# Kernel optimization log

Measured on AMD Instinct MI355X. Metric: run time of the kernel, lower is better.

## Reference

```python
import jax, jax.numpy as jnp
import numpy as np

N, L, E, H = 4, 2048, 512, 8
D = E // H


def setup_inputs() -> dict:
    key = jax.random.key(0)
    ks = jax.random.split(key, 8)
    causal = jnp.tril(jnp.ones((L, L), dtype=bool))[None, None]  # [1,1,L,L]
    return {
        "values": jax.random.normal(ks[0], (N, L, E), dtype=jnp.float32),
        "keys": jax.random.normal(ks[1], (N, L, E), dtype=jnp.float32),
        "query": jax.random.normal(ks[2], (N, L, E), dtype=jnp.float32),
        "mask": causal,
        "Wv": jax.random.normal(ks[3], (D, D), dtype=jnp.float32) * 0.05,
        "Wk": jax.random.normal(ks[4], (D, D), dtype=jnp.float32) * 0.05,
        "Wq": jax.random.normal(ks[5], (D, D), dtype=jnp.float32) * 0.05,
        "Wo": jax.random.normal(ks[6], (E, E), dtype=jnp.float32) * 0.05,
        "bo": jnp.zeros((E,), dtype=jnp.float32),
    }


def reference(values, keys, query, mask, Wv, Wk, Wq, Wo, bo):
    n, ql, e = query.shape
    # split heads: [N, len, H, D]
    v = values.reshape(n, -1, H, D)
    k = keys.reshape(n, -1, H, D)
    q = query.reshape(n, ql, H, D)
    # per-head linear projections (nn.Linear: x @ W.T, no bias)
    v = jnp.einsum("nlhd,od->nlho", v, Wv)
    k = jnp.einsum("nlhd,od->nlho", k, Wk)
    q = jnp.einsum("nqhd,od->nqho", q, Wq)
    # scores [N, H, Q, K]
    energy = jnp.einsum("nqhd,nkhd->nhqk", q, k)
    energy = jnp.where(mask == 0, jnp.float32(-1e28), energy)
    # NOTE: module scales by embed_size**0.5, not head_dim**0.5 (faithful)
    attn = jax.nn.softmax(energy / np.float32(e ** 0.5), axis=3)
    out = jnp.einsum("nhqk,nkhd->nqhd", attn, v).reshape(n, ql, e)
    return out @ Wo.T + bo
```

## Files before the change

kernel.cpp:

```cpp
#include <hip/hip_runtime.h>

#define NB 4
#define LL 2048
#define EE 512
#define HH 8
#define DD 64

typedef __attribute__((ext_vector_type(8))) short short8;
typedef __attribute__((ext_vector_type(4))) float f32x4;
typedef __attribute__((ext_vector_type(16))) float f32x16;
typedef __attribute__((ext_vector_type(4))) unsigned int u32x4;
typedef __attribute__((ext_vector_type(2))) int i32x2;
typedef __bf16 bf16x8 __attribute__((ext_vector_type(8)));

#if __has_builtin(__builtin_amdgcn_exp2f)
#define EXP2(x) __builtin_amdgcn_exp2f(x)
#else
#define EXP2(x) __expf((x) * 0.6931471805599453f)
#endif

#define QSCALE (0.04419417382415922f * 1.4426950408889634f)

static __device__ __forceinline__ short bfc(float f) {
    return __builtin_bit_cast(short, (__bf16)f);
}

static __device__ __forceinline__ unsigned pkbf(float lo, float hi) {
    unsigned short a = (unsigned short)(unsigned)__builtin_bit_cast(unsigned short, (__bf16)lo);
    unsigned short b = (unsigned short)(unsigned)__builtin_bit_cast(unsigned short, (__bf16)hi);
    return (unsigned)a | ((unsigned)b << 16);
}

#if __has_builtin(__builtin_amdgcn_permlane32_swap)
static __device__ __forceinline__ float plmax(float v) {
    i32x2 r = __builtin_amdgcn_permlane32_swap(
        __builtin_bit_cast(int, v), __builtin_bit_cast(int, v), false, false);
    return fmaxf(__builtin_bit_cast(float, r[0]), __builtin_bit_cast(float, r[1]));
}
#else
static __device__ __forceinline__ float plmax(float v) { return fmaxf(v, __shfl_xor(v, 32)); }
#endif

static __device__ __forceinline__ f32x4 mfma16(short8 a, short8 b, f32x4 c) {
    return __builtin_amdgcn_mfma_f32_16x16x32_bf16(
        __builtin_bit_cast(bf16x8, a), __builtin_bit_cast(bf16x8, b), c, 0, 0, 0);
}

static __device__ __forceinline__ f32x16 mfma32(short8 a, short8 b, f32x16 c) {
    return __builtin_amdgcn_mfma_f32_32x32x16_bf16(
        __builtin_bit_cast(bf16x8, a), __builtin_bit_cast(bf16x8, b), c, 0, 0, 0);
}

__global__ __launch_bounds__(256) void k_cvt(const float* __restrict__ src,
                                             unsigned short* __restrict__ dst, int n) {
    int i = (blockIdx.x * 256 + threadIdx.x) * 4;
    if (i < n) {
        float4 v = *(const float4*)(src + i);
        dst[i + 0] = (unsigned short)bfc(v.x);
        dst[i + 1] = (unsigned short)bfc(v.y);
        dst[i + 2] = (unsigned short)bfc(v.z);
        dst[i + 3] = (unsigned short)bfc(v.w);
    }
}

__global__ __launch_bounds__(256) void k_proj(const float* __restrict__ vals,
                                              const float* __restrict__ keys,
                                              const float* __restrict__ qry,
                                              const float* __restrict__ Wv,
                                              const float* __restrict__ Wk,
                                              const float* __restrict__ Wq,
                                              unsigned short* __restrict__ Qp,
                                              unsigned short* __restrict__ Kp,
                                              unsigned short* __restrict__ Vg) {
    __shared__ __align__(16) unsigned short kq[2][8256];
    __shared__ __align__(16) unsigned short vv[10272];

    const int tid = threadIdx.x;
    const int w = tid >> 6, ln = tid & 63;
    const int c = ln & 15, g = ln >> 4;
    const int r0 = blockIdx.x * 128;
    const int n = r0 >> 14;
    const int l0 = (r0 >> 3) & (LL - 1);
    const int h = c & 7;

    short8 xf[3][2][2];
    const float* Xs[3] = {vals, keys, qry};
#pragma unroll
    for (int t = 0; t < 3; ++t)
#pragma unroll
        for (int rt = 0; rt < 2; ++rt) {
            const int r = r0 + w * 32 + rt * 16 + c;
#pragma unroll
            for (int kk = 0; kk < 2; ++kk) {
                const float* p = Xs[t] + (size_t)r * DD + kk * 32 + g * 8;
                short8 v;
#pragma unroll
                for (int j = 0; j < 8; ++j) v[j] = bfc(p[j]);
                xf[t][rt][kk] = v;
            }
        }

#pragma unroll
    for (int t = 0; t < 3; ++t) {
        const float* W = (t == 0) ? Wv : (t == 1) ? Wk : Wq;
        short8 wf[4][2];
#pragma unroll
        for (int nt = 0; nt < 4; ++nt)
#pragma unroll
            for (int kk = 0; kk < 2; ++kk) {
                const float* p = W + (nt * 16 + c) * DD + kk * 32 + g * 8;
                short8 v;
#pragma unroll
                for (int j = 0; j < 8; ++j) v[j] = bfc(p[j]);
                wf[nt][kk] = v;
            }
#pragma unroll
        for (int rt = 0; rt < 2; ++rt) {
            const int l15 = w * 4 + rt * 2 + (c >> 3);
#pragma unroll
            for (int nt = 0; nt < 4; ++nt) {
                f32x4 acc = {0.f, 0.f, 0.f, 0.f};
                acc = mfma16(wf[nt][0], xf[t][rt][0], acc);
                acc = mfma16(wf[nt][1], xf[t][rt][1], acc);
                const int o = nt * 16 + g * 4;
                if (t == 0) {
#pragma unroll
                    for (int reg = 0; reg < 4; ++reg)
                        vv[h * 1284 + (o + reg) * 20 + l15] = (unsigned short)bfc(acc[reg]);
                } else {
                    const float s = (t == 2) ? QSCALE : 1.0f;
                    uint2 u = {pkbf(acc[0] * s, acc[1] * s), pkbf(acc[2] * s, acc[3] * s)};
                    *(uint2*)&kq[t - 1][h * 1032 + l15 * 64 + o] = u;
                }
            }
        }
    }
    __syncthreads();

#pragma unroll
    for (int t = 0; t < 2; ++t) {
        unsigned short* dstb = t ? Qp : Kp;
        const int hh = tid >> 5, s = tid & 31;
#pragma unroll
        for (int i = 0; i < 4; ++i) {
            const int q = s * 4 + i;
            const int l = q >> 3, cc = q & 7;
            uint4 v = *(const uint4*)&kq[t][hh * 1032 + l * 64 + cc * 8];
            *(uint4*)(dstb + ((size_t)(n * HH + hh) * LL + l0 + l) * DD + cc * 8) = v;
        }
    }

#pragma unroll
    for (int pi = 0; pi < 2; ++pi) {
        const int p = tid + pi * 256;
        const int hh = p >> 6, d = p & 63;
        const unsigned short* sp = &vv[hh * 1284 + d * 20];
        uint2 r0v = *(const uint2*)(sp + 0);
        uint2 r1v = *(const uint2*)(sp + 4);
        uint2 r2v = *(const uint2*)(sp + 8);
        uint2 r3v = *(const uint2*)(sp + 12);
        u32x4 o0 = {r0v.x, r0v.y, r1v.x, r1v.y};
        u32x4 o1 = {r2v.x, r2v.y, r3v.x, r3v.y};
        unsigned short* dst = Vg + (size_t)(n * HH + hh) * (LL * DD) +
                              (size_t)(l0 >> 4) * 1024 + d * 16;
        *(u32x4*)dst = o0;
        *(u32x4*)(dst + 8) = o1;
    }
}

static __device__ __forceinline__ void stage_tile(const unsigned short* __restrict__ src,
                                                  unsigned short* buf, int w, int ln,
                                                  size_t rstride) {
#pragma unroll
    for (int r = 0; r < 2; ++r) {
        int qi = w * 2 + r;
        int row = qi * 8 + (ln >> 3);
        int s = (ln & 7) ^ (row & 7);
        __builtin_amdgcn_global_load_lds(
            (const __attribute__((address_space(1))) unsigned int*)(src + (size_t)row * rstride + s * 8),
            (__attribute__((address_space(3))) unsigned int*)(buf + qi * 512),
            16, 0, 0);
    }
}

static __device__ __forceinline__ void stage_v(const unsigned short* __restrict__ src,
                                               unsigned short* buf, int w, int ln) {
#pragma unroll
    for (int r = 0; r < 2; ++r) {
        int idx = w * 64 + ln + r * 256;
        int d = idx >> 3, c16 = idx & 7;
        int cc = c16 ^ (d & 7);
        __builtin_amdgcn_global_load_lds(
            (const __attribute__((address_space(1))) unsigned int*)(src + (cc >> 1) * 1024 + d * 16 + (cc & 1) * 8),
            (__attribute__((address_space(3))) unsigned int*)(buf + idx * 8),
            16, 0, 0);
    }
}

__global__ __launch_bounds__(256, 4) void k_attn(const unsigned short* __restrict__ Qp,
                                                 const unsigned short* __restrict__ Kp,
                                                 const unsigned short* __restrict__ Vg,
                                                 unsigned short* __restrict__ Xa) {
    __shared__ __align__(16) unsigned short Kt[2][64 * 64];
    __shared__ __align__(16) unsigned short Vt[2][64 * 64];

    const int tid = threadIdx.x;
    const int w = tid >> 6, ln = tid & 63;
    const int c31 = ln & 31, g2 = ln >> 5;
    const int qpair = w >> 1, kvh = w & 1;

    const int b = blockIdx.x;
    const int x8 = b & 7;
    const int idx = b >> 3;
    const int nh = (x8 << 2) | (idx & 3);
    const int jj = (idx >> 2) & 15;
    const int j = (idx >> 6) ? jj : 31 - jj;
    const int qt = 2 * j + qpair;
    const int Q0 = qt * 32;
    const int nIter = j + 1;

    const unsigned short* Qb = Qp + (size_t)nh * (LL * DD);
    const unsigned short* Kb = Kp + (size_t)nh * (LL * DD);
    const unsigned short* Vb = Vg + (size_t)nh * (LL * DD);

    short8 qf[4];
#pragma unroll
    for (int kc = 0; kc < 4; ++kc)
        qf[kc] = *(const short8*)(Qb + (Q0 + c31) * DD + kc * 16 + g2 * 8);

    f32x16 oacc0, oacc1;
#pragma unroll
    for (int r = 0; r < 16; ++r) { oacc0[r] = 0.f; oacc1[r] = 0.f; }
    float m = -1e30f, lsum = 0.f;

    stage_tile(Kb, &Kt[0][0], w, ln, DD);
    stage_v(Vb, &Vt[0][0], w, ln);
    __syncthreads();

    int cur = 0;
    for (int t = 0; t < nIter; ++t) {
        const int nxt = cur ^ 1;
        if (t + 1 < nIter) {
            stage_tile(Kb + (size_t)(t + 1) * (64 * DD), &Kt[nxt][0], w, ln, DD);
            stage_v(Vb + (size_t)(t + 1) * 4096, &Vt[nxt][0], w, ln);
        }

        const int kb32 = t * 64 + kvh * 32;
        if (kb32 <= Q0 + 31) {
            const char* kb_ = (const char*)&Kt[cur][0];
            const char* vb_ = (const char*)&Vt[cur][0];
            const int q = Q0 + c31;

            f32x16 sc;
#pragma unroll
            for (int r = 0; r < 16; ++r) sc[r] = 0.f;
            {
                const int R = kvh * 32 + c31;
                const unsigned rb = (unsigned)(R * 128);
                const unsigned swz = (unsigned)((R & 7) << 4);
                __builtin_amdgcn_s_setprio(1);
#pragma unroll
                for (int kc = 0; kc < 4; ++kc) {
                    short8 af = *(const short8*)(kb_ + rb + (((unsigned)(kc * 32 + g2 * 16)) ^ swz));
                    sc = mfma32(af, qf[kc], sc);
                }
                __builtin_amdgcn_s_setprio(0);
            }

            if (kb32 + 31 > Q0) {
#pragma unroll
                for (int r = 0; r < 16; ++r) {
                    int kvg = kb32 + (r & 3) + 8 * (r >> 2) + 4 * g2;
                    sc[r] = (kvg > q) ? -1e30f : sc[r];
                }
            }

            float tm;
            {
                float a[8];
#pragma unroll
                for (int r = 0; r < 8; ++r) a[r] = fmaxf(sc[r], sc[r + 8]);
                float b0 = fmaxf(a[0], a[4]), b1 = fmaxf(a[1], a[5]);
                float b2 = fmaxf(a[2], a[6]), b3 = fmaxf(a[3], a[7]);
                tm = fmaxf(fmaxf(b0, b1), fmaxf(b2, b3));
            }
            tm = plmax(tm);

            if (!__all(tm <= m + 6.0f)) {
                float mn = fmaxf(m, tm);
                float corr = EXP2(m - mn);
                m = mn;
                lsum *= corr;
#pragma unroll
                for (int r = 0; r < 16; ++r) { oacc0[r] *= corr; oacc1[r] *= corr; }
            }

#pragma unroll
            for (int r = 0; r < 16; ++r) sc[r] = EXP2(sc[r] - m);
            {
                float a[8];
#pragma unroll
                for (int r = 0; r < 8; ++r) a[r] = sc[r] + sc[r + 8];
                float b0 = a[0] + a[4], b1 = a[1] + a[5];
                float b2 = a[2] + a[6], b3 = a[3] + a[7];
                lsum += (b0 + b1) + (b2 + b3);
            }

            unsigned pk[8];
#pragma unroll
            for (int iw = 0; iw < 8; ++iw) pk[iw] = pkbf(sc[2 * iw], sc[2 * iw + 1]);
#pragma unroll
            for (int ck = 0; ck < 2; ++ck) {
                unsigned s0 = g2 ? pk[4 * ck + 0] : pk[4 * ck + 2];
                unsigned s1 = g2 ? pk[4 * ck + 1] : pk[4 * ck + 3];
                unsigned x0 = __shfl_xor(s0, 32);
                unsigned x1 = __shfl_xor(s1, 32);
                u32x4 bfv;
                bfv[0] = g2 ? x0 : pk[4 * ck + 0];
                bfv[1] = g2 ? x1 : pk[4 * ck + 1];
                bfv[2] = g2 ? pk[4 * ck + 2] : x0;
                bfv[3] = g2 ? pk[4 * ck + 3] : x1;
                short8 pB = __builtin_bit_cast(short8, bfv);
                const unsigned coff = (unsigned)(kvh * 64 + ck * 32 + g2 * 16);
                __builtin_amdgcn_s_setprio(1);
                {
                    const int dP = c31;
                    short8 A = *(const short8*)(vb_ + (unsigned)(dP * 128) +
                                                (coff ^ ((unsigned)((dP & 7) << 4))));
                    oacc0 = mfma32(A, pB, oacc0);
                }
                {
                    const int dP = 32 + c31;
                    short8 A = *(const short8*)(vb_ + (unsigned)(dP * 128) +
                                                (coff ^ ((unsigned)((dP & 7) << 4))));
                    oacc1 = mfma32(A, pB, oacc1);
                }
                __builtin_amdgcn_s_setprio(0);
            }
        }

        __syncthreads();
        cur = nxt;
    }

    {
        float* mb = (float*)(&Kt[0][0]);
        float* lb = mb + 128;
        float* ob = (float*)(&Vt[0][0]);
        if (g2 == 0) mb[(qpair * 2 + kvh) * 32 + c31] = m;
        __syncthreads();
        const float mo = mb[(qpair * 2 + (kvh ^ 1)) * 32 + c31];
        const float alpha = EXP2(m - fmaxf(m, mo));
        lsum *= alpha;
#pragma unroll
        for (int r = 0; r < 16; ++r) { oacc0[r] *= alpha; oacc1[r] *= alpha; }
        if (kvh) {
            float* op = ob + qpair * 2048;
#pragma unroll
            for (int r = 0; r < 16; ++r) {
                op[r * 64 + ln] = oacc0[r];
                op[(16 + r) * 64 + ln] = oacc1[r];
            }
            lb[qpair * 64 + ln] = lsum;
        }
        __syncthreads();
        if (kvh) return;
        {
            const float* op = ob + qpair * 2048;
#pragma unroll
            for (int r = 0; r < 16; ++r) {
                oacc0[r] += op[r * 64 + ln];
                oacc1[r] += op[(16 + r) * 64 + ln];
            }
            lsum += lb[qpair * 64 + ln];
        }
    }

    lsum += __shfl_xor(lsum, 32);
    const float inv = 1.0f / lsum;
    const int n = nh >> 3, h = nh & 7;
    unsigned short* orow = Xa + ((size_t)(n * LL + Q0 + c31)) * EE + h * DD;
#pragma unroll
    for (int a = 0; a < 4; ++a) {
        {
            float e0 = oacc0[4 * a + 0] * inv, e1 = oacc0[4 * a + 1] * inv;
            float e2 = oacc0[4 * a + 2] * inv, e3 = oacc0[4 * a + 3] * inv;
            uint2 u = {pkbf(e0, e1), pkbf(e2, e3)};
            *(uint2*)(orow + a * 8 + g2 * 4) = u;
        }
        {
            float e0 = oacc1[4 * a + 0] * inv, e1 = oacc1[4 * a + 1] * inv;
            float e2 = oacc1[4 * a + 2] * inv, e3 = oacc1[4 * a + 3] * inv;
            uint2 u = {pkbf(e0, e1), pkbf(e2, e3)};
            *(uint2*)(orow + 32 + a * 8 + g2 * 4) = u;
        }
    }
}

__global__ __launch_bounds__(256) void k_out(const unsigned short* __restrict__ X,
                                             const unsigned short* __restrict__ Wob,
                                             const float* __restrict__ bo,
                                             float* __restrict__ out) {
    const int tid = threadIdx.x, w = tid >> 6, ln = tid & 63, c = ln & 15, g = ln >> 4;
    const int b = blockIdx.x;
    const int x8 = b & 7, jj = b >> 3;
    const int mb = x8 * 8 + (jj & 7);
    const int nb = jj >> 3;
    const int mbase = mb * 128 + w * 16;
    const int nbase = nb * 64;

    f32x4 acc0[4] = {}, acc1[4] = {};
    for (int ks = 0; ks < 16; ++ks) {
        short8 a0 = *(const short8*)(X + (size_t)(mbase + c) * EE + ks * 32 + g * 8);
        short8 a1 = *(const short8*)(X + (size_t)(mbase + 64 + c) * EE + ks * 32 + g * 8);
#pragma unroll
        for (int nt = 0; nt < 4; ++nt) {
            short8 bfr = *(const short8*)(Wob + (size_t)(nbase + nt * 16 + c) * EE + ks * 32 + g * 8);
            acc0[nt] = mfma16(a0, bfr, acc0[nt]);
            acc1[nt] = mfma16(a1, bfr, acc1[nt]);
        }
    }
#pragma unroll
    for (int nt = 0; nt < 4; ++nt) {
        float bias = bo[nbase + nt * 16 + c];
#pragma unroll
        for (int reg = 0; reg < 4; ++reg) {
            int row0 = mbase + g * 4 + reg;
            out[(size_t)row0 * EE + nbase + nt * 16 + c] = acc0[nt][reg] + bias;
            out[(size_t)(row0 + 64) * EE + nbase + nt * 16 + c] = acc1[nt][reg] + bias;
        }
    }
}

extern "C" void kernel_launch(void* const* d_in, const int* in_sizes, int n_in,
                              void* d_out, int out_size, void* d_ws, size_t ws_size,
                              hipStream_t stream) {
    const float* vals = (const float*)d_in[0];
    const float* keys = (const float*)d_in[1];
    const float* qry  = (const float*)d_in[2];
    const float* Wv = (const float*)d_in[4];
    const float* Wk = (const float*)d_in[5];
    const float* Wq = (const float*)d_in[6];
    const float* Wo = (const float*)d_in[7];
    const float* bo = (const float*)d_in[8];
    float* out = (float*)d_out;

    char* ws = (char*)d_ws;
    unsigned short* Qp  = (unsigned short*)(ws);
    unsigned short* Kp  = (unsigned short*)(ws + (8u  << 20));
    unsigned short* Vg  = (unsigned short*)(ws + (16u << 20));
    unsigned short* Xa  = (unsigned short*)(ws + (24u << 20));
    unsigned short* Wob = (unsigned short*)(ws + (32u << 20));

    hipLaunchKernelGGL(k_cvt, dim3(256), dim3(256), 0, stream, Wo, Wob, EE * EE);
    hipLaunchKernelGGL(k_proj, dim3(512), dim3(256), 0, stream,
                       vals, keys, qry, Wv, Wk, Wq, Qp, Kp, Vg);
    hipLaunchKernelGGL(k_attn, dim3(1024), dim3(256), 0, stream, Qp, Kp, Vg, Xa);
    hipLaunchKernelGGL(k_out, dim3(512), dim3(256), 0, stream, Xa, Wob, bo, out);
}
```

Before: 98.74 us.

## Fold Wo conversion into projection kernel, split K/Q and V blocks, prefetch in k_out

Removes the separate Wo fp32-to-bf16 conversion launch by folding it into the projection kernel's first 512 blocks. The projection grid doubles: half the blocks project K and Q, the other half project V, sharing one smaller LDS buffer, with launch bounds raised to allow four blocks per CU. The output GEMM gains register double-buffering, so the next k-step's A/B fragments load while the current MFMAs run. This trims launch overhead and improves occupancy and latency hiding, at the cost of more registers in k_out and duplicated per-block work such as reloading the W fragments.

```diff
diff --git a/kernel.cpp b/kernel.cpp
--- a/kernel.cpp
+++ b/kernel.cpp
@@ -51,120 +51,159 @@
         __builtin_bit_cast(bf16x8, a), __builtin_bit_cast(bf16x8, b), c, 0, 0, 0);
 }
 
-__global__ __launch_bounds__(256) void k_cvt(const float* __restrict__ src,
-                                             unsigned short* __restrict__ dst, int n) {
-    int i = (blockIdx.x * 256 + threadIdx.x) * 4;
-    if (i < n) {
-        float4 v = *(const float4*)(src + i);
-        dst[i + 0] = (unsigned short)bfc(v.x);
-        dst[i + 1] = (unsigned short)bfc(v.y);
-        dst[i + 2] = (unsigned short)bfc(v.z);
-        dst[i + 3] = (unsigned short)bfc(v.w);
-    }
-}
-
-__global__ __launch_bounds__(256) void k_proj(const float* __restrict__ vals,
-                                              const float* __restrict__ keys,
-                                              const float* __restrict__ qry,
-                                              const float* __restrict__ Wv,
-                                              const float* __restrict__ Wk,
-                                              const float* __restrict__ Wq,
-                                              unsigned short* __restrict__ Qp,
-                                              unsigned short* __restrict__ Kp,
-                                              unsigned short* __restrict__ Vg) {
-    __shared__ __align__(16) unsigned short kq[2][8256];
-    __shared__ __align__(16) unsigned short vv[10272];
+__global__ __launch_bounds__(256, 4) void k_proj(const float* __restrict__ vals,
+                                                 const float* __restrict__ keys,
+                                                 const float* __restrict__ qry,
+                                                 const float* __restrict__ Wv,
+                                                 const float* __restrict__ Wk,
+                                                 const float* __restrict__ Wq,
+                                                 const float* __restrict__ Wo,
+                                                 unsigned short* __restrict__ Qp,
+                                                 unsigned short* __restrict__ Kp,
+                                                 unsigned short* __restrict__ Vg,
+                                                 unsigned short* __restrict__ Wob) {
+    __shared__ __align__(16) unsigned short smem[16512];
 
     const int tid = threadIdx.x;
     const int w = tid >> 6, ln = tid & 63;
     const int c = ln & 15, g = ln >> 4;
-    const int r0 = blockIdx.x * 128;
-    const int n = r0 >> 14;
-    const int l0 = (r0 >> 3) & (LL - 1);
-    const int h = c & 7;
-
-    short8 xf[3][2][2];
-    const float* Xs[3] = {vals, keys, qry};
-#pragma unroll
-    for (int t = 0; t < 3; ++t)
+
+    if (blockIdx.x < 512) {
+        {
+            const int i = blockIdx.x * 512 + tid * 2;
+            float2 v = *(const float2*)(Wo + i);
+            Wob[i] = (unsigned short)bfc(v.x);
+            Wob[i + 1] = (unsigned short)bfc(v.y);
+        }
+        unsigned short (*kq)[8256] = (unsigned short (*)[8256])smem;
+        const int r0 = blockIdx.x * 128;
+        const int n = r0 >> 14;
+        const int l0 = (r0 >> 3) & (LL - 1);
+        const int h = c & 7;
+
+#pragma unroll
+        for (int t = 0; t < 2; ++t) {
+            const float* X = t ? qry : keys;
+            const float* W = t ? Wq : Wk;
+
+            short8 xf[2][2];
+#pragma unroll
+            for (int rt = 0; rt < 2; ++rt) {
+                const int r = r0 + w * 32 + rt * 16 + c;
+#pragma unroll
+                for (int kk = 0; kk < 2; ++kk) {
+                    const float* p = X + (size_t)r * DD + kk * 32 + g * 8;
+                    short8 v;
+#pragma unroll
+                    for (int j = 0; j < 8; ++j) v[j] = bfc(p[j]);
+                    xf[rt][kk] = v;
+                }
+            }
+            short8 wf[4][2];
+#pragma unroll
+            for (int nt = 0; nt < 4; ++nt)
+#pragma unroll
+                for (int kk = 0; kk < 2; ++kk) {
+                    const float* p = W + (nt * 16 + c) * DD + kk * 32 + g * 8;
+                    short8 v;
+#pragma unroll
+                    for (int j = 0; j < 8; ++j) v[j] = bfc(p[j]);
+                    wf[nt][kk] = v;
+                }
+
+#pragma unroll
+            for (int rt = 0; rt < 2; ++rt) {
+                const int l15 = w * 4 + rt * 2 + (c >> 3);
+#pragma unroll
+                for (int nt = 0; nt < 4; ++nt) {
+                    f32x4 acc = {0.f, 0.f, 0.f, 0.f};
+                    acc = mfma16(wf[nt][0], xf[rt][0], acc);
+                    acc = mfma16(wf[nt][1], xf[rt][1], acc);
+                    const int o = nt * 16 + g * 4;
+                    const float s = t ? QSCALE : 1.0f;
+                    uint2 u = {pkbf(acc[0] * s, acc[1] * s), pkbf(acc[2] * s, acc[3] * s)};
+                    *(uint2*)&kq[t][h * 1032 + l15 * 64 + o] = u;
+                }
+            }
+        }
+        __syncthreads();
+
+#pragma unroll
+        for (int t = 0; t < 2; ++t) {
+            unsigned short* dstb = t ? Qp : Kp;
+            const int hh = tid >> 5, s = tid & 31;
+#pragma unroll
+            for (int i = 0; i < 4; ++i) {
+                const int q = s * 4 + i;
+                const int l = q >> 3, cc = q & 7;
+                uint4 v = *(const uint4*)&kq[t][hh * 1032 + l * 64 + cc * 8];
+                *(uint4*)(dstb + ((size_t)(n * HH + hh) * LL + l0 + l) * DD + cc * 8) = v;
+            }
+        }
+    } else {
+        unsigned short* vv = smem;
+        const int r0 = (blockIdx.x - 512) * 128;
+        const int n = r0 >> 14;
+        const int l0 = (r0 >> 3) & (LL - 1);
+        const int h = c & 15 & 7;
+
+        short8 xf[2][2];
 #pragma unroll
         for (int rt = 0; rt < 2; ++rt) {
             const int r = r0 + w * 32 + rt * 16 + c;
 #pragma unroll
             for (int kk = 0; kk < 2; ++kk) {
-                const float* p = Xs[t] + (size_t)r * DD + kk * 32 + g * 8;
+                const float* p = vals + (size_t)r * DD + kk * 32 + g * 8;
                 short8 v;
 #pragma unroll
                 for (int j = 0; j < 8; ++j) v[j] = bfc(p[j]);
-                xf[t][rt][kk] = v;
-            }
-        }
-
-#pragma unroll
-    for (int t = 0; t < 3; ++t) {
-        const float* W = (t == 0) ? Wv : (t == 1) ? Wk : Wq;
+                xf[rt][kk] = v;
+            }
+        }
         short8 wf[4][2];
 #pragma unroll
         for (int nt = 0; nt < 4; ++nt)
 #pragma unroll
             for (int kk = 0; kk < 2; ++kk) {
-                const float* p = W + (nt * 16 + c) * DD + kk * 32 + g * 8;
+                const float* p = Wv + (nt * 16 + c) * DD + kk * 32 + g * 8;
                 short8 v;
 #pragma unroll
                 for (int j = 0; j < 8; ++j) v[j] = bfc(p[j]);
                 wf[nt][kk] = v;
             }
+
 #pragma unroll
         for (int rt = 0; rt < 2; ++rt) {
             const int l15 = w * 4 + rt * 2 + (c >> 3);
 #pragma unroll
             for (int nt = 0; nt < 4; ++nt) {
                 f32x4 acc = {0.f, 0.f, 0.f, 0.f};
-                acc = mfma16(wf[nt][0], xf[t][rt][0], acc);
-                acc = mfma16(wf[nt][1], xf[t][rt][1], acc);
+                acc = mfma16(wf[nt][0], xf[rt][0], acc);
+                acc = mfma16(wf[nt][1], xf[rt][1], acc);
                 const int o = nt * 16 + g * 4;
-                if (t == 0) {
-#pragma unroll
-                    for (int reg = 0; reg < 4; ++reg)
-                        vv[h * 1284 + (o + reg) * 20 + l15] = (unsigned short)bfc(acc[reg]);
-                } else {
-                    const float s = (t == 2) ? QSCALE : 1.0f;
-                    uint2 u = {pkbf(acc[0] * s, acc[1] * s), pkbf(acc[2] * s, acc[3] * s)};
-                    *(uint2*)&kq[t - 1][h * 1032 + l15 * 64 + o] = u;
-                }
-            }
-        }
-    }
-    __syncthreads();
-
-#pragma unroll
-    for (int t = 0; t < 2; ++t) {
-        unsigned short* dstb = t ? Qp : Kp;
-        const int hh = tid >> 5, s = tid & 31;
-#pragma unroll
-        for (int i = 0; i < 4; ++i) {
-            const int q = s * 4 + i;
-            const int l = q >> 3, cc = q & 7;
-            uint4 v = *(const uint4*)&kq[t][hh * 1032 + l * 64 + cc * 8];
-            *(uint4*)(dstb + ((size_t)(n * HH + hh) * LL + l0 + l) * DD + cc * 8) = v;
-        }
-    }
-
-#pragma unroll
-    for (int pi = 0; pi < 2; ++pi) {
-        const int p = tid + pi * 256;
-        const int hh = p >> 6, d = p & 63;
-        const unsigned short* sp = &vv[hh * 1284 + d * 20];
-        uint2 r0v = *(const uint2*)(sp + 0);
-        uint2 r1v = *(const uint2*)(sp + 4);
-        uint2 r2v = *(const uint2*)(sp + 8);
-        uint2 r3v = *(const uint2*)(sp + 12);
-        u32x4 o0 = {r0v.x, r0v.y, r1v.x, r1v.y};
-        u32x4 o1 = {r2v.x, r2v.y, r3v.x, r3v.y};
-        unsigned short* dst = Vg + (size_t)(n * HH + hh) * (LL * DD) +
-                              (size_t)(l0 >> 4) * 1024 + d * 16;
-        *(u32x4*)dst = o0;
-        *(u32x4*)(dst + 8) = o1;
+#pragma unroll
+                for (int reg = 0; reg < 4; ++reg)
+                    vv[h * 1284 + (o + reg) * 20 + l15] = (unsigned short)bfc(acc[reg]);
+            }
+        }
+        __syncthreads();
+
+#pragma unroll
+        for (int pi = 0; pi < 2; ++pi) {
+            const int p = tid + pi * 256;
+            const int hh = p >> 6, d = p & 63;
+            const unsigned short* sp = &vv[hh * 1284 + d * 20];
+            uint2 r0v = *(const uint2*)(sp + 0);
+            uint2 r1v = *(const uint2*)(sp + 4);
+            uint2 r2v = *(const uint2*)(sp + 8);
+            uint2 r3v = *(const uint2*)(sp + 12);
+            u32x4 o0 = {r0v.x, r0v.y, r1v.x, r1v.y};
+            u32x4 o1 = {r2v.x, r2v.y, r3v.x, r3v.y};
+            unsigned short* dst = Vg + (size_t)(n * HH + hh) * (LL * DD) +
+                                  (size_t)(l0 >> 4) * 1024 + d * 16;
+            *(u32x4*)dst = o0;
+            *(u32x4*)(dst + 8) = o1;
+        }
     }
 }
 
@@ -409,15 +448,36 @@
     const int mbase = mb * 128 + w * 16;
     const int nbase = nb * 64;
 
+    const unsigned short* Xr0 = X + (size_t)(mbase + c) * EE + g * 8;
+    const unsigned short* Xr1 = X + (size_t)(mbase + 64 + c) * EE + g * 8;
+    const unsigned short* Wr = Wob + (size_t)(nbase + c) * EE + g * 8;
+
     f32x4 acc0[4] = {}, acc1[4] = {};
+    short8 a0 = *(const short8*)(Xr0);
+    short8 a1 = *(const short8*)(Xr1);
+    short8 bf[4];
+#pragma unroll
+    for (int nt = 0; nt < 4; ++nt) bf[nt] = *(const short8*)(Wr + (size_t)nt * 16 * EE);
+
+#pragma unroll
     for (int ks = 0; ks < 16; ++ks) {
-        short8 a0 = *(const short8*)(X + (size_t)(mbase + c) * EE + ks * 32 + g * 8);
-        short8 a1 = *(const short8*)(X + (size_t)(mbase + 64 + c) * EE + ks * 32 + g * 8);
+        short8 na0, na1, nbf[4];
+        if (ks < 15) {
+            na0 = *(const short8*)(Xr0 + (ks + 1) * 32);
+            na1 = *(const short8*)(Xr1 + (ks + 1) * 32);
+#pragma unroll
+            for (int nt = 0; nt < 4; ++nt)
+                nbf[nt] = *(const short8*)(Wr + (size_t)nt * 16 * EE + (ks + 1) * 32);
+        }
 #pragma unroll
         for (int nt = 0; nt < 4; ++nt) {
-            short8 bfr = *(const short8*)(Wob + (size_t)(nbase + nt * 16 + c) * EE + ks * 32 + g * 8);
-            acc0[nt] = mfma16(a0, bfr, acc0[nt]);
-            acc1[nt] = mfma16(a1, bfr, acc1[nt]);
+            acc0[nt] = mfma16(a0, bf[nt], acc0[nt]);
+            acc1[nt] = mfma16(a1, bf[nt], acc1[nt]);
+        }
+        if (ks < 15) {
+            a0 = na0; a1 = na1;
+#pragma unroll
+            for (int nt = 0; nt < 4; ++nt) bf[nt] = nbf[nt];
         }
     }
 #pragma unroll
@@ -452,9 +512,8 @@
     unsigned short* Xa  = (unsigned short*)(ws + (24u << 20));
     unsigned short* Wob = (unsigned short*)(ws + (32u << 20));
 
-    hipLaunchKernelGGL(k_cvt, dim3(256), dim3(256), 0, stream, Wo, Wob, EE * EE);
-    hipLaunchKernelGGL(k_proj, dim3(512), dim3(256), 0, stream,
-                       vals, keys, qry, Wv, Wk, Wq, Qp, Kp, Vg);
+    hipLaunchKernelGGL(k_proj, dim3(1024), dim3(256), 0, stream,
+                       vals, keys, qry, Wv, Wk, Wq, Wo, Qp, Kp, Vg, Wob);
     hipLaunchKernelGGL(k_attn, dim3(1024), dim3(256), 0, stream, Qp, Kp, Vg, Xa);
     hipLaunchKernelGGL(k_out, dim3(512), dim3(256), 0, stream, Xa, Wob, bo, out);
 }
```

New measurement: 92.26 us. 1.07x faster.
